# Kernel optimization log

Measured on AMD Instinct MI355X. Metric: run time of the kernel, lower is better.

## Reference

```python
import jax, jax.numpy as jnp
import numpy as np

EPS = 1e-5


def conv1x1(x, w, b=None):
    # x: [B,C,H,W], w: [O,C] (1x1 conv kernel squeezed)
    y = jnp.einsum('bchw,oc->bohw', x, w)
    if b is not None:
        y = y + b[None, :, None, None]
    return y


def bn_inf(x, g, b, m, v):
    scale = g / jnp.sqrt(v + EPS)
    return (x - m[None, :, None, None]) * scale[None, :, None, None] + b[None, :, None, None]


def setup_inputs() -> dict:
    B, C, H, W = 2, 256, 80, 80
    Ck, Cv, Co = 64, 128, 256
    key = jax.random.key(0)
    ks = jax.random.split(key, 16)
    d = {}
    d['x'] = jax.random.normal(ks[0], (B, C, H, W), dtype=jnp.float32)
    d['y'] = jax.random.normal(ks[1], (B, C, H, W), dtype=jnp.float32)
    s = 1.0 / np.sqrt(C)
    d['fk_w'] = jax.random.normal(ks[2], (Ck, C), dtype=jnp.float32) * s
    d['fk_g'] = jnp.ones((Ck,), jnp.float32)
    d['fk_b'] = jnp.zeros((Ck,), jnp.float32)
    d['fk_m'] = jax.random.normal(ks[3], (Ck,), dtype=jnp.float32) * 0.1
    d['fk_v'] = jax.random.uniform(ks[4], (Ck,), minval=0.5, maxval=1.5, dtype=jnp.float32)
    d['fq_w'] = jax.random.normal(ks[5], (Ck, C), dtype=jnp.float32) * s
    d['fq_g'] = jnp.ones((Ck,), jnp.float32)
    d['fq_b'] = jnp.zeros((Ck,), jnp.float32)
    d['fq_m'] = jax.random.normal(ks[6], (Ck,), dtype=jnp.float32) * 0.1
    d['fq_v'] = jax.random.uniform(ks[7], (Ck,), minval=0.5, maxval=1.5, dtype=jnp.float32)
    d['fv_w'] = jax.random.normal(ks[8], (Cv, C), dtype=jnp.float32) * s
    d['fv_b'] = jnp.zeros((Cv,), jnp.float32)
    d['W_w'] = jax.random.normal(ks[9], (Co, Cv), dtype=jnp.float32) * (1.0 / np.sqrt(Cv))
    d['W_b'] = jnp.zeros((Co,), jnp.float32)
    d['gamma'] = jnp.array([0.5], jnp.float32)
    return d


def reference(x, y, fk_w, fk_g, fk_b, fk_m, fk_v, fq_w, fq_g, fq_b, fq_m, fq_v, fv_w, fv_b, W_w, W_b, gamma):
    B, C, H, W = x.shape
    Ck = fk_w.shape[0]
    Cv = fv_w.shape[0]
    N = H * W
    # key from x, query/value from y (1x1 conv + BN projections)
    k = bn_inf(conv1x1(x, fk_w), fk_g, fk_b, fk_m, fk_v).reshape(B, Ck, N)          # [B,Ck,N]
    q = bn_inf(conv1x1(y, fq_w), fq_g, fq_b, fq_m, fq_v).reshape(B, Ck, N)          # [B,Ck,N]
    v = conv1x1(y, fv_w, fv_b).reshape(B, Cv, N)                                     # [B,Cv,N]
    sim = jnp.einsum('bkn,bkm->bnm', q, k) * (Ck ** -0.5)                            # [B,N,N]
    sim = jax.nn.softmax(sim, axis=-1)
    ctx = jnp.einsum('bnm,bvm->bvn', sim, v).reshape(B, Cv, H, W)                    # [B,Cv,H,W]
    ctx = conv1x1(ctx, W_w, W_b)                                                     # [B,Co,H,W]
    return gamma[0] * ctx + x
```

## Files before the change

### kernel.cpp

```cpp
#include <hip/hip_runtime.h>
#include <math.h>

#define NB   2
#define CIN  256
#define NN   6400
#define CKd  64
#define CVd  128
#define COd  256

using bf16   = __bf16;
using bf16x4 = __attribute__((ext_vector_type(4))) bf16;
using bf16x8 = __attribute__((ext_vector_type(8))) bf16;
using f32x4  = __attribute__((ext_vector_type(4))) float;

__device__ __forceinline__ void lds_cp16(const bf16* g, bf16* l) {
    __builtin_amdgcn_global_load_lds((const __attribute__((address_space(1))) void*)g,
                                     (__attribute__((address_space(3))) void*)l, 16, 0, 0);
}

__global__ void prep_kernel(const float* __restrict__ fk_w, const float* __restrict__ fk_g,
                            const float* __restrict__ fk_b, const float* __restrict__ fk_m,
                            const float* __restrict__ fk_v,
                            const float* __restrict__ fq_w, const float* __restrict__ fq_g,
                            const float* __restrict__ fq_b, const float* __restrict__ fq_m,
                            const float* __restrict__ fq_v,
                            const float* __restrict__ fv_w, const float* __restrict__ fv_b,
                            const float* __restrict__ W_w,  const float* __restrict__ W_b,
                            bf16* __restrict__ wkb, bf16* __restrict__ wqb,
                            bf16* __restrict__ wvb, bf16* __restrict__ wob,
                            float* __restrict__ bias)
{
    const int idx = blockIdx.x * 256 + threadIdx.x;
    if (idx < 16384) {
        const int co = idx >> 8;
        const float a = fk_g[co] * rsqrtf(fk_v[co] + 1e-5f);
        wkb[idx] = (bf16)(fk_w[idx] * a);
    } else if (idx < 32768) {
        const int i = idx - 16384, co = i >> 8;
        const float a = fq_g[co] * rsqrtf(fq_v[co] + 1e-5f) * 0.125f;
        wqb[i] = (bf16)(fq_w[i] * a);
    } else if (idx < 65536) {
        const int i = idx - 32768;
        wvb[i] = (bf16)fv_w[i];
    } else if (idx < 98304) {
        const int i = idx - 65536;
        wob[i] = (bf16)W_w[i];
    } else if (idx < 98816) {
        const int j = idx - 98304;
        if (j < 64)       { const float a = fk_g[j] * rsqrtf(fk_v[j] + 1e-5f); bias[j] = fk_b[j] - fk_m[j] * a; }
        else if (j < 128) { const int c = j - 64; const float a = fq_g[c] * rsqrtf(fq_v[c] + 1e-5f); bias[j] = (fq_b[c] - fq_m[c] * a) * 0.125f; }
        else if (j < 256) bias[j] = fv_b[j - 128];
        else              bias[j] = W_b[j - 256];
    }
}

__launch_bounds__(256)
__global__ void tcvt_kernel(const float* __restrict__ x, const float* __restrict__ y,
                            bf16* __restrict__ xT, bf16* __restrict__ yT)
{
    __shared__ __align__(16) bf16 t_lds[64][68];
    const int b = blockIdx.z & 1;
    const float* src = (blockIdx.z >> 1) ? y : x;
    bf16* dst = (blockIdx.z >> 1) ? yT : xT;
    const int n0 = blockIdx.x * 64, c0 = blockIdx.y * 64;
    const int tid = threadIdx.x;
    const int nl = (tid & 15) * 4;
#pragma unroll
    for (int p = 0; p < 4; ++p) {
        const int cl = (tid >> 4) + p * 16;
        const float4 v = *(const float4*)(src + (size_t)(b * CIN + c0 + cl) * NN + n0 + nl);
        t_lds[nl + 0][cl] = (bf16)v.x;
        t_lds[nl + 1][cl] = (bf16)v.y;
        t_lds[nl + 2][cl] = (bf16)v.z;
        t_lds[nl + 3][cl] = (bf16)v.w;
    }
    __syncthreads();
#pragma unroll
    for (int p = 0; p < 4; ++p) {
        const int u = tid + p * 256;
        const int n = u >> 4, c4 = (u & 15) * 4;
        const bf16x4 pk = *(const bf16x4*)&t_lds[n][c4];
        *(bf16x4*)(dst + ((size_t)b * NN + n0 + n) * CIN + c0 + c4) = pk;
    }
}

__launch_bounds__(256, 4)
__global__ void projkqv_kernel(const bf16* __restrict__ xT, const bf16* __restrict__ yT,
                               const bf16* __restrict__ wkb, const bf16* __restrict__ wqb,
                               const bf16* __restrict__ wvb, const float* __restrict__ bias,
                               bf16* __restrict__ kb, bf16* __restrict__ qb, bf16* __restrict__ vb)
{
    const int tid  = threadIdx.x;
    const int lane = tid & 63, wav = tid >> 6;
    const int l15  = lane & 15, quad = lane >> 4;
    const int b    = blockIdx.z, m = blockIdx.y;

    if (m < 2) {
        const bf16* src = (m == 0) ? xT : yT;
        const bf16* w   = (m == 0) ? wkb : wqb;
        const float* bs = bias + m * 64;
        bf16* dst       = (m == 0) ? kb : qb;
        const int n0 = blockIdx.x * 64 + wav * 16;

        f32x4 acc[4];
#pragma unroll
        for (int j = 0; j < 4; ++j) acc[j] = (f32x4){0.f, 0.f, 0.f, 0.f};

        for (int kk = 0; kk < CIN; kk += 32) {
            const bf16x8 af = *(const bf16x8*)(src + ((size_t)b * NN + n0 + l15) * CIN + kk + quad * 8);
#pragma unroll
            for (int nt = 0; nt < 4; ++nt) {
                const bf16x8 bfw = *(const bf16x8*)(w + (size_t)(nt * 16 + l15) * CIN + kk + quad * 8);
                acc[nt] = __builtin_amdgcn_mfma_f32_16x16x32_bf16(af, bfw, acc[nt], 0, 0, 0);
            }
        }
#pragma unroll
        for (int nt = 0; nt < 4; ++nt) {
            const float bv = bs[nt * 16 + l15];
#pragma unroll
            for (int r = 0; r < 4; ++r) {
                const int n = n0 + quad * 4 + r;
                dst[((size_t)b * NN + n) * CKd + nt * 16 + l15] = (bf16)(acc[nt][r] + bv);
            }
        }
    } else {
        const int cv0 = (m - 2) * 64 + wav * 16;
        const int nb0 = blockIdx.x * 64;

        f32x4 acc[4];
#pragma unroll
        for (int j = 0; j < 4; ++j) acc[j] = (f32x4){0.f, 0.f, 0.f, 0.f};

        for (int kk = 0; kk < CIN; kk += 32) {
            const bf16x8 af = *(const bf16x8*)(wvb + (size_t)(cv0 + l15) * CIN + kk + quad * 8);
#pragma unroll
            for (int nt = 0; nt < 4; ++nt) {
                const bf16x8 bfy = *(const bf16x8*)(yT + ((size_t)b * NN + nb0 + nt * 16 + l15) * CIN + kk + quad * 8);
                acc[nt] = __builtin_amdgcn_mfma_f32_16x16x32_bf16(af, bfy, acc[nt], 0, 0, 0);
            }
        }
#pragma unroll
        for (int r = 0; r < 4; ++r) {
            const int cv = cv0 + quad * 4 + r;
            const float bv = bias[128 + cv];
#pragma unroll
            for (int nt = 0; nt < 4; ++nt)
                vb[((size_t)b * CVd + cv) * NN + nb0 + nt * 16 + l15] = (bf16)(acc[nt][r] + bv);
        }
    }
}

__launch_bounds__(256, 3)
__global__ void attn_kernel(const bf16* __restrict__ qb, const bf16* __restrict__ kb,
                            const bf16* __restrict__ vb,
                            bf16* __restrict__ pO, float* __restrict__ pl, int tpc)
{
    __shared__ __align__(16) bf16 kbuf[64 * 64];
    __shared__ __align__(16) bf16 vbuf[128 * 64];
    __shared__ __align__(16) bf16 p_lds[4][2][16][72];

    const int lane = threadIdx.x & 63;
    const int wav  = threadIdx.x >> 6;
    const int l15  = lane & 15;
    const int quad = lane >> 4;
    const int r8   = lane >> 3;
    const int c_st = lane & 7;
    const int c_src = c_st ^ r8;
    const int sw   = l15 & 7;
    const int b    = blockIdx.y;
    const int q0   = blockIdx.x * 128 + wav * 32;

    const bf16* qrow = qb + (size_t)b * NN * CKd;
    const bf16* krow = kb + (size_t)b * NN * CKd;
    const bf16* vrow = vb + (size_t)b * CVd * NN;

    bf16x8 qf[2][2];
#pragma unroll
    for (int qt = 0; qt < 2; ++qt)
#pragma unroll
        for (int s = 0; s < 2; ++s)
            qf[qt][s] = *(const bf16x8*)(qrow + (size_t)(q0 + qt * 16 + l15) * CKd + s * 32 + quad * 8);

    f32x4 acc[2][8];
#pragma unroll
    for (int qt = 0; qt < 2; ++qt)
#pragma unroll
        for (int cv = 0; cv < 8; ++cv) acc[qt][cv] = (f32x4){0.f, 0.f, 0.f, 0.f};
    float psum[2] = {0.f, 0.f};

    const int t0  = blockIdx.z * tpc;
    const int rem = 100 - t0;
    const int nt  = (tpc < rem) ? tpc : rem;

    for (int t = 0; t < nt; ++t) {
        const int key0 = (t0 + t) * 64;

        __syncthreads();
        lds_cp16(krow + (size_t)(key0 + wav * 8 + r8) * CKd + c_src * 8,
                 &kbuf[(wav * 8) * 64]);
        lds_cp16(krow + (size_t)(key0 + (wav + 4) * 8 + r8) * CKd + c_src * 8,
                 &kbuf[((wav + 4) * 8) * 64]);
#pragma unroll
        for (int g4 = 0; g4 < 4; ++g4) {
            const int g = wav * 4 + g4;
            lds_cp16(vrow + (size_t)(g * 8 + r8) * NN + key0 + c_src * 8,
                     &vbuf[(g * 8) * 64]);
        }
        __syncthreads();

        f32x4 s4[2][4];
#pragma unroll
        for (int kt = 0; kt < 4; ++kt) {
            const int rr = kt * 16 + l15;
            const bf16x8 kf0 = *(const bf16x8*)&kbuf[rr * 64 + ((quad ^ sw) * 8)];
            const bf16x8 kf1 = *(const bf16x8*)&kbuf[rr * 64 + (((4 + quad) ^ sw) * 8)];
#pragma unroll
            for (int qt = 0; qt < 2; ++qt) {
                f32x4 z = (f32x4){0.f, 0.f, 0.f, 0.f};
                z = __builtin_amdgcn_mfma_f32_16x16x32_bf16(kf0, qf[qt][0], z, 0, 0, 0);
                z = __builtin_amdgcn_mfma_f32_16x16x32_bf16(kf1, qf[qt][1], z, 0, 0, 0);
                s4[qt][kt] = z;
            }
        }

#pragma unroll
        for (int qt = 0; qt < 2; ++qt) {
            float ps = 0.f;
#pragma unroll
            for (int kt = 0; kt < 4; ++kt) {
                bf16x4 pk;
#pragma unroll
                for (int r = 0; r < 4; ++r) {
                    const float p = exp2f(fmaf(s4[qt][kt][r], 1.4426950408889634f, -11.541560327111707f));
                    ps += p;
                    pk[r] = (bf16)p;
                }
                *(bf16x4*)&p_lds[wav][qt][l15][kt * 16 + quad * 4] = pk;
            }
            psum[qt] += ps;
        }

        bf16x8 pf[2][2];
#pragma unroll
        for (int qt = 0; qt < 2; ++qt)
#pragma unroll
            for (int sp = 0; sp < 2; ++sp)
                pf[qt][sp] = *(const bf16x8*)&p_lds[wav][qt][l15][sp * 32 + quad * 8];

#pragma unroll
        for (int sp = 0; sp < 2; ++sp)
#pragma unroll
            for (int cvt = 0; cvt < 8; ++cvt) {
                const int rr = cvt * 16 + l15;
                const bf16x8 vf = *(const bf16x8*)&vbuf[rr * 64 + (((sp * 4 + quad) ^ sw) * 8)];
                acc[0][cvt] = __builtin_amdgcn_mfma_f32_16x16x32_bf16(vf, pf[0][sp], acc[0][cvt], 0, 0, 0);
                acc[1][cvt] = __builtin_amdgcn_mfma_f32_16x16x32_bf16(vf, pf[1][sp], acc[1][cvt], 0, 0, 0);
            }
    }

    const size_t pb = (size_t)blockIdx.z * NB + b;
#pragma unroll
    for (int qt = 0; qt < 2; ++qt) {
        psum[qt] += __shfl_xor(psum[qt], 16);
        psum[qt] += __shfl_xor(psum[qt], 32);
        const int qa = q0 + qt * 16 + l15;
#pragma unroll
        for (int cvt = 0; cvt < 8; ++cvt) {
            bf16x4 pk;
#pragma unroll
            for (int r = 0; r < 4; ++r) pk[r] = (bf16)acc[qt][cvt][r];
            *(bf16x4*)(pO + (pb * NN + qa) * CVd + cvt * 16 + quad * 4) = pk;
        }
        if (quad == 0) pl[pb * NN + qa] = psum[qt];
    }
}

__global__ void combine_kernel(const bf16* __restrict__ pO, const float* __restrict__ pl,
                               bf16* __restrict__ ctxT, int KS)
{
    const int idx = blockIdx.x * 256 + threadIdx.x;
    const int c4  = (idx & 31) * 4;
    const int rest = idx >> 5;
    const int n = rest % NN, b = rest / NN;

    float v0 = 0.f, v1 = 0.f, v2 = 0.f, v3 = 0.f, L = 0.f;
    for (int ks = 0; ks < KS; ++ks) {
        const size_t base = (size_t)(ks * NB + b) * NN + n;
        const bf16x4 tv = *(const bf16x4*)(pO + base * CVd + c4);
        v0 += (float)tv[0]; v1 += (float)tv[1]; v2 += (float)tv[2]; v3 += (float)tv[3];
        L += pl[base];
    }
    const float r = 1.0f / L;
    bf16x4 o;
    o[0] = (bf16)(v0 * r); o[1] = (bf16)(v1 * r); o[2] = (bf16)(v2 * r); o[3] = (bf16)(v3 * r);
    *(bf16x4*)(ctxT + ((size_t)b * NN + n) * CVd + c4) = o;
}

__launch_bounds__(256, 4)
__global__ void outproj_kernel(const bf16* __restrict__ ctxT, const bf16* __restrict__ wob,
                               const float* __restrict__ bias, const float* __restrict__ x,
                               const float* __restrict__ gam, float* __restrict__ out)
{
    const int tid  = threadIdx.x;
    const int lane = tid & 63, wav = tid >> 6;
    const int l15  = lane & 15, quad = lane >> 4;
    const int b    = blockIdx.z;
    const int co0  = blockIdx.y * 64 + wav * 16;
    const int n0   = blockIdx.x * 64;

    f32x4 acc[4];
#pragma unroll
    for (int j = 0; j < 4; ++j) acc[j] = (f32x4){0.f, 0.f, 0.f, 0.f};

    for (int kk = 0; kk < CVd; kk += 32) {
        const bf16x8 af = *(const bf16x8*)(wob + (size_t)(co0 + l15) * CVd + kk + quad * 8);
#pragma unroll
        for (int nt = 0; nt < 4; ++nt) {
            const bf16x8 bfc = *(const bf16x8*)(ctxT + ((size_t)b * NN + n0 + nt * 16 + l15) * CVd + kk + quad * 8);
            acc[nt] = __builtin_amdgcn_mfma_f32_16x16x32_bf16(af, bfc, acc[nt], 0, 0, 0);
        }
    }

    const float gm = gam[0];
#pragma unroll
    for (int r = 0; r < 4; ++r) {
        const int co = co0 + quad * 4 + r;
        const float bv = bias[256 + co];
#pragma unroll
        for (int nt = 0; nt < 4; ++nt) {
            const int n = n0 + nt * 16 + l15;
            const size_t a = ((size_t)b * COd + co) * NN + n;
            out[a] = gm * (acc[nt][r] + bv) + x[a];
        }
    }
}

extern "C" void kernel_launch(void* const* d_in, const int* in_sizes, int n_in,
                              void* d_out, int out_size, void* d_ws, size_t ws_size,
                              hipStream_t stream)
{
    const float* x     = (const float*)d_in[0];
    const float* y     = (const float*)d_in[1];
    const float* fk_w  = (const float*)d_in[2];
    const float* fk_g  = (const float*)d_in[3];
    const float* fk_b  = (const float*)d_in[4];
    const float* fk_m  = (const float*)d_in[5];
    const float* fk_v  = (const float*)d_in[6];
    const float* fq_w  = (const float*)d_in[7];
    const float* fq_g  = (const float*)d_in[8];
    const float* fq_b  = (const float*)d_in[9];
    const float* fq_m  = (const float*)d_in[10];
    const float* fq_v  = (const float*)d_in[11];
    const float* fv_w  = (const float*)d_in[12];
    const float* fv_b  = (const float*)d_in[13];
    const float* W_w   = (const float*)d_in[14];
    const float* W_b   = (const float*)d_in[15];
    const float* gamma = (const float*)d_in[16];
    float* out = (float*)d_out;

    char* ws = (char*)d_ws;
    size_t off = 0;
    auto carve = [&](size_t bytes) -> char* {
        char* p = ws + off;
        off = (off + bytes + 255) & ~(size_t)255;
        return p;
    };

    bf16*  kb   = (bf16*)carve((size_t)NB * NN * CKd * 2);
    bf16*  qbuf = (bf16*)carve((size_t)NB * NN * CKd * 2);
    bf16*  vb   = (bf16*)carve((size_t)NB * CVd * NN * 2);
    bf16*  wkb  = (bf16*)carve((size_t)CKd * CIN * 2);
    bf16*  wqb  = (bf16*)carve((size_t)CKd * CIN * 2);
    bf16*  wvb  = (bf16*)carve((size_t)CVd * CIN * 2);
    bf16*  wob  = (bf16*)carve((size_t)COd * CVd * 2);
    float* bias = (float*)carve(512 * 4);
    bf16*  ctxT = (bf16*)carve((size_t)NB * NN * CVd * 2);

    const size_t alias_start = off;
    bf16* xT = (bf16*)carve((size_t)NB * NN * CIN * 2);
    bf16* yT = (bf16*)carve((size_t)NB * NN * CIN * 2);

    const size_t region = ws_size - alias_start;
    const size_t per_ks = (size_t)NB * NN * CVd * 2 + (size_t)NB * NN * 4 + 512;
    int KS = 1;
    {
        const int cand[6] = {10, 8, 5, 4, 2, 1};
        for (int i = 0; i < 6; ++i)
            if ((size_t)cand[i] * per_ks <= region) { KS = cand[i]; break; }
    }
    bf16*  pO = (bf16*)(ws + alias_start);
    float* pl = (float*)(ws + alias_start + (size_t)KS * NB * NN * CVd * 2);
    const int tpc = (100 + KS - 1) / KS;

    const dim3 blk(256);
    prep_kernel<<<386, blk, 0, stream>>>(fk_w, fk_g, fk_b, fk_m, fk_v,
                                         fq_w, fq_g, fq_b, fq_m, fq_v,
                                         fv_w, fv_b, W_w, W_b,
                                         wkb, wqb, wvb, wob, bias);
    tcvt_kernel<<<dim3(100, 4, 4), blk, 0, stream>>>(x, y, xT, yT);
    projkqv_kernel<<<dim3(100, 4, NB), blk, 0, stream>>>(xT, yT, wkb, wqb, wvb, bias, kb, qbuf, vb);
    attn_kernel<<<dim3(50, NB, KS), blk, 0, stream>>>(qbuf, kb, vb, pO, pl, tpc);
    combine_kernel<<<dim3((NB * NN * CVd / 4) / 256), blk, 0, stream>>>(pO, pl, ctxT, KS);
    outproj_kernel<<<dim3(100, 4, NB), blk, 0, stream>>>(ctxT, wob, bias, x, gamma, out);
}
```

Before: 198.2 us.

## Stage projection tiles in LDS and swizzle attention P buffer

The projection kernel now copies the whole 64x256 activation tile and weight tile into shared memory with direct global-to-LDS loads and an XOR swizzle, then runs the MFMA loop from LDS instead of re-reading global memory per wave. The attention kernel drops the padded P scratch layout for an XOR-swizzled unpadded one, shrinking LDS so the launch bound can rise from 3 to 4 blocks per SM. The projection kernel's occupancy hint drops to 2 because it now uses 64 KB of LDS per block.

```diff
diff --git a/kernel.cpp b/kernel.cpp
--- a/kernel.cpp
+++ b/kernel.cpp
@@ -84,80 +84,97 @@
     }
 }
 
-__launch_bounds__(256, 4)
+__launch_bounds__(256, 2)
 __global__ void projkqv_kernel(const bf16* __restrict__ xT, const bf16* __restrict__ yT,
                                const bf16* __restrict__ wkb, const bf16* __restrict__ wqb,
                                const bf16* __restrict__ wvb, const float* __restrict__ bias,
                                bf16* __restrict__ kb, bf16* __restrict__ qb, bf16* __restrict__ vb)
 {
+    __shared__ __align__(16) bf16 sbuf[64 * 256];
+    __shared__ __align__(16) bf16 wbuf[64 * 256];
+
     const int tid  = threadIdx.x;
     const int lane = tid & 63, wav = tid >> 6;
     const int l15  = lane & 15, quad = lane >> 4;
     const int b    = blockIdx.z, m = blockIdx.y;
+    const int n0   = blockIdx.x * 64;
+
+    const bf16* srcg = ((m == 0) ? xT : yT) + ((size_t)b * NN + n0) * CIN;
+    const bf16* wg   = (m == 0) ? wkb : (m == 1) ? wqb : (wvb + (size_t)(m - 2) * 64 * CIN);
+
+    const int r2  = lane >> 5;
+    const int c32 = lane & 31;
+#pragma unroll
+    for (int i = 0; i < 8; ++i) {
+        const int rg = wav * 16 + i * 2;
+        const int r  = rg + r2;
+        const int cs = c32 ^ (r & 7);
+        lds_cp16(srcg + (size_t)r * 256 + cs * 8, &sbuf[rg * 256]);
+        lds_cp16(wg   + (size_t)r * 256 + cs * 8, &wbuf[rg * 256]);
+    }
+    __syncthreads();
+
+    const int key = l15 & 7;
+    f32x4 acc[4];
+#pragma unroll
+    for (int j = 0; j < 4; ++j) acc[j] = (f32x4){0.f, 0.f, 0.f, 0.f};
 
     if (m < 2) {
-        const bf16* src = (m == 0) ? xT : yT;
-        const bf16* w   = (m == 0) ? wkb : wqb;
+        const int arow = wav * 16 + l15;
+#pragma unroll
+        for (int k4 = 0; k4 < 32; k4 += 4) {
+            const bf16x8 af = *(const bf16x8*)&sbuf[arow * 256 + ((k4 + quad) ^ key) * 8];
+#pragma unroll
+            for (int nt = 0; nt < 4; ++nt) {
+                const int brow = nt * 16 + l15;
+                const bf16x8 bfw = *(const bf16x8*)&wbuf[brow * 256 + ((k4 + quad) ^ key) * 8];
+                acc[nt] = __builtin_amdgcn_mfma_f32_16x16x32_bf16(af, bfw, acc[nt], 0, 0, 0);
+            }
+        }
         const float* bs = bias + m * 64;
-        bf16* dst       = (m == 0) ? kb : qb;
-        const int n0 = blockIdx.x * 64 + wav * 16;
-
-        f32x4 acc[4];
-#pragma unroll
-        for (int j = 0; j < 4; ++j) acc[j] = (f32x4){0.f, 0.f, 0.f, 0.f};
-
-        for (int kk = 0; kk < CIN; kk += 32) {
-            const bf16x8 af = *(const bf16x8*)(src + ((size_t)b * NN + n0 + l15) * CIN + kk + quad * 8);
-#pragma unroll
-            for (int nt = 0; nt < 4; ++nt) {
-                const bf16x8 bfw = *(const bf16x8*)(w + (size_t)(nt * 16 + l15) * CIN + kk + quad * 8);
-                acc[nt] = __builtin_amdgcn_mfma_f32_16x16x32_bf16(af, bfw, acc[nt], 0, 0, 0);
-            }
-        }
+        bf16* dst = (m == 0) ? kb : qb;
+        const int nb = n0 + wav * 16;
 #pragma unroll
         for (int nt = 0; nt < 4; ++nt) {
             const float bv = bs[nt * 16 + l15];
 #pragma unroll
             for (int r = 0; r < 4; ++r) {
-                const int n = n0 + quad * 4 + r;
+                const int n = nb + quad * 4 + r;
                 dst[((size_t)b * NN + n) * CKd + nt * 16 + l15] = (bf16)(acc[nt][r] + bv);
             }
         }
     } else {
+        const int arow = wav * 16 + l15;
+#pragma unroll
+        for (int k4 = 0; k4 < 32; k4 += 4) {
+            const bf16x8 af = *(const bf16x8*)&wbuf[arow * 256 + ((k4 + quad) ^ key) * 8];
+#pragma unroll
+            for (int nt = 0; nt < 4; ++nt) {
+                const int brow = nt * 16 + l15;
+                const bf16x8 bfy = *(const bf16x8*)&sbuf[brow * 256 + ((k4 + quad) ^ key) * 8];
+                acc[nt] = __builtin_amdgcn_mfma_f32_16x16x32_bf16(af, bfy, acc[nt], 0, 0, 0);
+            }
+        }
         const int cv0 = (m - 2) * 64 + wav * 16;
-        const int nb0 = blockIdx.x * 64;
-
-        f32x4 acc[4];
-#pragma unroll
-        for (int j = 0; j < 4; ++j) acc[j] = (f32x4){0.f, 0.f, 0.f, 0.f};
-
-        for (int kk = 0; kk < CIN; kk += 32) {
-            const bf16x8 af = *(const bf16x8*)(wvb + (size_t)(cv0 + l15) * CIN + kk + quad * 8);
-#pragma unroll
-            for (int nt = 0; nt < 4; ++nt) {
-                const bf16x8 bfy = *(const bf16x8*)(yT + ((size_t)b * NN + nb0 + nt * 16 + l15) * CIN + kk + quad * 8);
-                acc[nt] = __builtin_amdgcn_mfma_f32_16x16x32_bf16(af, bfy, acc[nt], 0, 0, 0);
-            }
-        }
 #pragma unroll
         for (int r = 0; r < 4; ++r) {
             const int cv = cv0 + quad * 4 + r;
             const float bv = bias[128 + cv];
 #pragma unroll
             for (int nt = 0; nt < 4; ++nt)
-                vb[((size_t)b * CVd + cv) * NN + nb0 + nt * 16 + l15] = (bf16)(acc[nt][r] + bv);
-        }
-    }
-}
-
-__launch_bounds__(256, 3)
+                vb[((size_t)b * CVd + cv) * NN + n0 + nt * 16 + l15] = (bf16)(acc[nt][r] + bv);
+        }
+    }
+}
+
+__launch_bounds__(256, 4)
 __global__ void attn_kernel(const bf16* __restrict__ qb, const bf16* __restrict__ kb,
                             const bf16* __restrict__ vb,
                             bf16* __restrict__ pO, float* __restrict__ pl, int tpc)
 {
     __shared__ __align__(16) bf16 kbuf[64 * 64];
     __shared__ __align__(16) bf16 vbuf[128 * 64];
-    __shared__ __align__(16) bf16 p_lds[4][2][16][72];
+    __shared__ __align__(16) bf16 p_lds[4][2][16][64];
 
     const int lane = threadIdx.x & 63;
     const int wav  = threadIdx.x >> 6;
@@ -167,6 +184,7 @@
     const int c_st = lane & 7;
     const int c_src = c_st ^ r8;
     const int sw   = l15 & 7;
+    const int pkey = (l15 & 7) << 1;
     const int b    = blockIdx.y;
     const int q0   = blockIdx.x * 128 + wav * 32;
 
@@ -235,7 +253,7 @@
                     ps += p;
                     pk[r] = (bf16)p;
                 }
-                *(bf16x4*)&p_lds[wav][qt][l15][kt * 16 + quad * 4] = pk;
+                *(bf16x4*)&p_lds[wav][qt][l15][((kt * 4 + quad) ^ pkey) * 4] = pk;
             }
             psum[qt] += ps;
         }
@@ -245,7 +263,7 @@
         for (int qt = 0; qt < 2; ++qt)
 #pragma unroll
             for (int sp = 0; sp < 2; ++sp)
-                pf[qt][sp] = *(const bf16x8*)&p_lds[wav][qt][l15][sp * 32 + quad * 8];
+                pf[qt][sp] = *(const bf16x8*)&p_lds[wav][qt][l15][((sp * 8 + quad * 2) ^ pkey) * 4];
 
 #pragma unroll
         for (int sp = 0; sp < 2; ++sp)
```

Measured after the change: 236.5 us. 1.19x slower.
